# Kernel tuning notes

Hardware: AMD Instinct MI355X
Metric: run time of the kernel (lower is better)

The kernel has to match this reference:

```python
import jax, jax.numpy as jnp
import numpy as np

B, S1, S2, H, H2, D, K = 1, 1024, 8192, 32, 8, 128, 128


def setup_inputs() -> dict:
    key = jax.random.key(0)
    k1, k2, k3, k4 = jax.random.split(key, 4)
    q = jax.random.normal(k1, (B, S1, H, D), dtype=jnp.float16)
    k = jax.random.normal(k2, (B, S2, H2, D), dtype=jnp.float16)
    v = jax.random.normal(k3, (B, S2, H2, D), dtype=jnp.float16)
    sparse_indices = jax.random.randint(k4, (B, S1, H2, K), 0, S2, dtype=jnp.int32)
    return {"q": q, "k": k, "v": v, "sparse_indices": sparse_indices}


def reference(q, k, v, sparse_indices):
    # q: [B,S1,H,D]  k,v: [B,S2,H2,D]  sparse_indices: [B,S1,H2,K]
    b, s1, h, d = q.shape
    h2 = sparse_indices.shape[2]
    g = h // h2  # GQA group size
    scale = 1.0 / np.sqrt(d).astype(np.float32)
    qg = q.reshape(b, s1, h2, g, d)  # group queries per kv head
    b_idx = jnp.arange(b)[:, None, None, None]
    h_idx = jnp.arange(h2)[None, None, :, None]
    # gather per-query sparse KV sets: [B,S1,H2,K,D]
    kg = k[b_idx, sparse_indices, h_idx]
    vg = v[b_idx, sparse_indices, h_idx]
    scores = jnp.einsum('bshgd,bshkd->bshgk', qg, kg).astype(jnp.float32) * scale
    p = jax.nn.softmax(scores, axis=-1).astype(q.dtype)
    out = jnp.einsum('bshgk,bshkd->bshgd', p, vg)  # [B,S1,H2,G,D]
    return out.reshape(b, s1, h, d).astype(jnp.float16)
```

## Files before the change

### kernel.cpp

```cpp
#include <hip/hip_runtime.h>
#include <stdint.h>
#include <math.h>

#define NH 32
#define NH2 8
#define DD 128
#define KSEL 128
#define GG 4
#define S2MASK 8191

__global__ __launch_bounds__(256) void sparse_attn_kernel(
    const float* __restrict__ q, const float* __restrict__ k,
    const float* __restrict__ v, const int* __restrict__ idx,
    float* __restrict__ out) {
  __shared__ int sIdx[4][KSEL];
  __shared__ __align__(16) float sS[4][GG][KSEL];
  __shared__ __align__(16) float sP[4][KSEL][GG];

  const int tid = threadIdx.x;
  const int w = tid >> 6;
  const int lane = tid & 63;
  const int h2 = blockIdx.x & 7;
  const int s1 = ((blockIdx.x >> 3) << 2) + w;

  const int* ip = idx + (s1 * NH2 + h2) * KSEL;
  sIdx[w][lane]      = ip[lane] & S2MASK;
  sIdx[w][lane + 64] = ip[lane + 64] & S2MASK;

  const int c = lane & 15;
  const int r = lane >> 4;
  float4 qa[GG], qb[GG];
  const float* qp = q + (s1 * NH + h2 * GG) * DD + c * 8;
#pragma unroll
  for (int g = 0; g < GG; ++g) {
    qa[g] = *(const float4*)(qp + g * DD);
    qb[g] = *(const float4*)(qp + g * DD + 4);
  }

  __syncthreads();

  const float scale = 0.08838834764831845f;

#pragma unroll 4
  for (int it = 0; it < 32; ++it) {
    const int j = it * 4 + r;
    const int s2 = sIdx[w][j];
    const float* kp = k + (s2 * NH2 + h2) * DD + c * 8;
    const float4 ka = *(const float4*)(kp);
    const float4 kb = *(const float4*)(kp + 4);
    float sg0, sg1, sg2, sg3;
    {
      sg0 = qa[0].x * ka.x; sg1 = qa[1].x * ka.x;
      sg2 = qa[2].x * ka.x; sg3 = qa[3].x * ka.x;
      sg0 = fmaf(qa[0].y, ka.y, sg0); sg1 = fmaf(qa[1].y, ka.y, sg1);
      sg2 = fmaf(qa[2].y, ka.y, sg2); sg3 = fmaf(qa[3].y, ka.y, sg3);
      sg0 = fmaf(qa[0].z, ka.z, sg0); sg1 = fmaf(qa[1].z, ka.z, sg1);
      sg2 = fmaf(qa[2].z, ka.z, sg2); sg3 = fmaf(qa[3].z, ka.z, sg3);
      sg0 = fmaf(qa[0].w, ka.w, sg0); sg1 = fmaf(qa[1].w, ka.w, sg1);
      sg2 = fmaf(qa[2].w, ka.w, sg2); sg3 = fmaf(qa[3].w, ka.w, sg3);
      sg0 = fmaf(qb[0].x, kb.x, sg0); sg1 = fmaf(qb[1].x, kb.x, sg1);
      sg2 = fmaf(qb[2].x, kb.x, sg2); sg3 = fmaf(qb[3].x, kb.x, sg3);
      sg0 = fmaf(qb[0].y, kb.y, sg0); sg1 = fmaf(qb[1].y, kb.y, sg1);
      sg2 = fmaf(qb[2].y, kb.y, sg2); sg3 = fmaf(qb[3].y, kb.y, sg3);
      sg0 = fmaf(qb[0].z, kb.z, sg0); sg1 = fmaf(qb[1].z, kb.z, sg1);
      sg2 = fmaf(qb[2].z, kb.z, sg2); sg3 = fmaf(qb[3].z, kb.z, sg3);
      sg0 = fmaf(qb[0].w, kb.w, sg0); sg1 = fmaf(qb[1].w, kb.w, sg1);
      sg2 = fmaf(qb[2].w, kb.w, sg2); sg3 = fmaf(qb[3].w, kb.w, sg3);
    }
#pragma unroll
    for (int off = 1; off < 16; off <<= 1) {
      sg0 += __shfl_xor(sg0, off);
      sg1 += __shfl_xor(sg1, off);
      sg2 += __shfl_xor(sg2, off);
      sg3 += __shfl_xor(sg3, off);
    }
    float val = (c == 0) ? sg0 : (c == 1) ? sg1 : (c == 2) ? sg2 : sg3;
    if (c < GG) sS[w][c][j] = val * scale;
  }
  __syncthreads();

#pragma unroll
  for (int g = 0; g < GG; ++g) {
    float a0 = sS[w][g][lane];
    float a1 = sS[w][g][lane + 64];
    float m = fmaxf(a0, a1);
#pragma unroll
    for (int off = 32; off >= 1; off >>= 1) m = fmaxf(m, __shfl_xor(m, off));
    float e0 = expf(a0 - m);
    float e1 = expf(a1 - m);
    float s = e0 + e1;
#pragma unroll
    for (int off = 32; off >= 1; off >>= 1) s += __shfl_xor(s, off);
    const float inv = 1.0f / fmaxf(s, 1e-30f);
    sP[w][lane][g]      = e0 * inv;
    sP[w][lane + 64][g] = e1 * inv;
  }
  __syncthreads();

  float a00 = 0.f, a01 = 0.f, a10 = 0.f, a11 = 0.f;
  float a20 = 0.f, a21 = 0.f, a30 = 0.f, a31 = 0.f;
  const float* vb = v + h2 * DD + lane * 2;
#pragma unroll 8
  for (int j = 0; j < KSEL; ++j) {
    const int s2 = sIdx[w][j];
    const float2 vv = *(const float2*)(vb + (size_t)s2 * (NH2 * DD));
    const float4 p = *(const float4*)&sP[w][j][0];
    a00 = fmaf(p.x, vv.x, a00); a01 = fmaf(p.x, vv.y, a01);
    a10 = fmaf(p.y, vv.x, a10); a11 = fmaf(p.y, vv.y, a11);
    a20 = fmaf(p.z, vv.x, a20); a21 = fmaf(p.z, vv.y, a21);
    a30 = fmaf(p.w, vv.x, a30); a31 = fmaf(p.w, vv.y, a31);
  }

  float* op = out + (s1 * NH + h2 * GG) * DD + lane * 2;
  *(float2*)(op + 0 * DD) = make_float2(a00, a01);
  *(float2*)(op + 1 * DD) = make_float2(a10, a11);
  *(float2*)(op + 2 * DD) = make_float2(a20, a21);
  *(float2*)(op + 3 * DD) = make_float2(a30, a31);
}

extern "C" void kernel_launch(void* const* d_in, const int* in_sizes, int n_in,
                              void* d_out, int out_size, void* d_ws, size_t ws_size,
                              hipStream_t stream) {
  const float* q = (const float*)d_in[0];
  const float* k = (const float*)d_in[1];
  const float* v = (const float*)d_in[2];
  const int* idx = (const int*)d_in[3];
  float* out = (float*)d_out;
  sparse_attn_kernel<<<dim3(2048), dim3(256), 0, stream>>>(q, k, v, idx, out);
}
```

Before: 183.9 us.

## Compute QK scores with fp16 MFMA and vectorize softmax across group heads

Replaces the scalar FMA plus shuffle-reduction QK dot products with 16x16x32 fp16 MFMA instructions. Q (padded to 16 rows, only 4 used) and the gathered K rows are converted from fp32 to fp16 in registers. Scores are written straight into the sP buffer, which removes the separate sS array. The softmax now processes all four group heads at once with float4 and uses fast __expf. The change reduces ALU and shuffle work in the score phase, at the cost of wasted MFMA rows and fp16 rounding of K and Q.

```diff
diff --git a/kernel.cpp b/kernel.cpp
--- a/kernel.cpp
+++ b/kernel.cpp
@@ -9,12 +9,24 @@
 #define GG 4
 #define S2MASK 8191
 
+typedef _Float16 h8   __attribute__((ext_vector_type(8)));
+typedef __fp16   hp2  __attribute__((ext_vector_type(2)));
+typedef float    f32x4 __attribute__((ext_vector_type(4)));
+
+static __device__ __forceinline__ h8 cvt8(float4 a, float4 b) {
+  union { h8 v; hp2 p[4]; } u;
+  u.p[0] = __builtin_amdgcn_cvt_pkrtz(a.x, a.y);
+  u.p[1] = __builtin_amdgcn_cvt_pkrtz(a.z, a.w);
+  u.p[2] = __builtin_amdgcn_cvt_pkrtz(b.x, b.y);
+  u.p[3] = __builtin_amdgcn_cvt_pkrtz(b.z, b.w);
+  return u.v;
+}
+
 __global__ __launch_bounds__(256) void sparse_attn_kernel(
     const float* __restrict__ q, const float* __restrict__ k,
     const float* __restrict__ v, const int* __restrict__ idx,
     float* __restrict__ out) {
   __shared__ int sIdx[4][KSEL];
-  __shared__ __align__(16) float sS[4][GG][KSEL];
   __shared__ __align__(16) float sP[4][KSEL][GG];
 
   const int tid = threadIdx.x;
@@ -27,73 +39,77 @@
   sIdx[w][lane]      = ip[lane] & S2MASK;
   sIdx[w][lane + 64] = ip[lane + 64] & S2MASK;
 
-  const int c = lane & 15;
-  const int r = lane >> 4;
-  float4 qa[GG], qb[GG];
-  const float* qp = q + (s1 * NH + h2 * GG) * DD + c * 8;
+  const int m  = lane & 15;
+  const int kg = lane >> 4;
+
+  h8 aq[4];
 #pragma unroll
-  for (int g = 0; g < GG; ++g) {
-    qa[g] = *(const float4*)(qp + g * DD);
-    qb[g] = *(const float4*)(qp + g * DD + 4);
+  for (int t = 0; t < 4; ++t)
+#pragma unroll
+    for (int i = 0; i < 8; ++i) aq[t][i] = (_Float16)0;
+  if (m < GG) {
+    const float* qp = q + (s1 * NH + h2 * GG + m) * DD + kg * 8;
+#pragma unroll
+    for (int t = 0; t < 4; ++t) {
+      float4 f0 = *(const float4*)(qp + 32 * t);
+      float4 f1 = *(const float4*)(qp + 32 * t + 4);
+      aq[t] = cvt8(f0, f1);
+    }
   }
 
   __syncthreads();
 
   const float scale = 0.08838834764831845f;
 
-#pragma unroll 4
-  for (int it = 0; it < 32; ++it) {
-    const int j = it * 4 + r;
-    const int s2 = sIdx[w][j];
-    const float* kp = k + (s2 * NH2 + h2) * DD + c * 8;
-    const float4 ka = *(const float4*)(kp);
-    const float4 kb = *(const float4*)(kp + 4);
-    float sg0, sg1, sg2, sg3;
-    {
-      sg0 = qa[0].x * ka.x; sg1 = qa[1].x * ka.x;
-      sg2 = qa[2].x * ka.x; sg3 = qa[3].x * ka.x;
-      sg0 = fmaf(qa[0].y, ka.y, sg0); sg1 = fmaf(qa[1].y, ka.y, sg1);
-      sg2 = fmaf(qa[2].y, ka.y, sg2); sg3 = fmaf(qa[3].y, ka.y, sg3);
-      sg0 = fmaf(qa[0].z, ka.z, sg0); sg1 = fmaf(qa[1].z, ka.z, sg1);
-      sg2 = fmaf(qa[2].z, ka.z, sg2); sg3 = fmaf(qa[3].z, ka.z, sg3);
-      sg0 = fmaf(qa[0].w, ka.w, sg0); sg1 = fmaf(qa[1].w, ka.w, sg1);
-      sg2 = fmaf(qa[2].w, ka.w, sg2); sg3 = fmaf(qa[3].w, ka.w, sg3);
-      sg0 = fmaf(qb[0].x, kb.x, sg0); sg1 = fmaf(qb[1].x, kb.x, sg1);
-      sg2 = fmaf(qb[2].x, kb.x, sg2); sg3 = fmaf(qb[3].x, kb.x, sg3);
-      sg0 = fmaf(qb[0].y, kb.y, sg0); sg1 = fmaf(qb[1].y, kb.y, sg1);
-      sg2 = fmaf(qb[2].y, kb.y, sg2); sg3 = fmaf(qb[3].y, kb.y, sg3);
-      sg0 = fmaf(qb[0].z, kb.z, sg0); sg1 = fmaf(qb[1].z, kb.z, sg1);
-      sg2 = fmaf(qb[2].z, kb.z, sg2); sg3 = fmaf(qb[3].z, kb.z, sg3);
-      sg0 = fmaf(qb[0].w, kb.w, sg0); sg1 = fmaf(qb[1].w, kb.w, sg1);
-      sg2 = fmaf(qb[2].w, kb.w, sg2); sg3 = fmaf(qb[3].w, kb.w, sg3);
+#pragma unroll 2
+  for (int nt = 0; nt < 8; ++nt) {
+    const int s2 = sIdx[w][nt * 16 + m];
+    const float* kp = k + (s2 * NH2 + h2) * DD + kg * 8;
+    f32x4 acc = {0.f, 0.f, 0.f, 0.f};
+#pragma unroll
+    for (int t = 0; t < 4; ++t) {
+      float4 f0 = *(const float4*)(kp + 32 * t);
+      float4 f1 = *(const float4*)(kp + 32 * t + 4);
+      acc = __builtin_amdgcn_mfma_f32_16x16x32_f16(aq[t], cvt8(f0, f1), acc, 0, 0, 0);
     }
-#pragma unroll
-    for (int off = 1; off < 16; off <<= 1) {
-      sg0 += __shfl_xor(sg0, off);
-      sg1 += __shfl_xor(sg1, off);
-      sg2 += __shfl_xor(sg2, off);
-      sg3 += __shfl_xor(sg3, off);
+    if (lane < 16) {
+      float4 sc = make_float4(acc[0] * scale, acc[1] * scale,
+                              acc[2] * scale, acc[3] * scale);
+      *(float4*)&sP[w][nt * 16 + lane][0] = sc;
     }
-    float val = (c == 0) ? sg0 : (c == 1) ? sg1 : (c == 2) ? sg2 : sg3;
-    if (c < GG) sS[w][c][j] = val * scale;
   }
   __syncthreads();
 
+  {
+    float4 p0 = *(const float4*)&sP[w][lane][0];
+    float4 p1 = *(const float4*)&sP[w][lane + 64][0];
+    float4 mx = make_float4(fmaxf(p0.x, p1.x), fmaxf(p0.y, p1.y),
+                            fmaxf(p0.z, p1.z), fmaxf(p0.w, p1.w));
 #pragma unroll
-  for (int g = 0; g < GG; ++g) {
-    float a0 = sS[w][g][lane];
-    float a1 = sS[w][g][lane + 64];
-    float m = fmaxf(a0, a1);
+    for (int off = 1; off < 64; off <<= 1) {
+      mx.x = fmaxf(mx.x, __shfl_xor(mx.x, off));
+      mx.y = fmaxf(mx.y, __shfl_xor(mx.y, off));
+      mx.z = fmaxf(mx.z, __shfl_xor(mx.z, off));
+      mx.w = fmaxf(mx.w, __shfl_xor(mx.w, off));
+    }
+    float4 e0 = make_float4(__expf(p0.x - mx.x), __expf(p0.y - mx.y),
+                            __expf(p0.z - mx.z), __expf(p0.w - mx.w));
+    float4 e1 = make_float4(__expf(p1.x - mx.x), __expf(p1.y - mx.y),
+                            __expf(p1.z - mx.z), __expf(p1.w - mx.w));
+    float4 sm = make_float4(e0.x + e1.x, e0.y + e1.y, e0.z + e1.z, e0.w + e1.w);
 #pragma unroll
-    for (int off = 32; off >= 1; off >>= 1) m = fmaxf(m, __shfl_xor(m, off));
-    float e0 = expf(a0 - m);
-    float e1 = expf(a1 - m);
-    float s = e0 + e1;
-#pragma unroll
-    for (int off = 32; off >= 1; off >>= 1) s += __shfl_xor(s, off);
-    const float inv = 1.0f / fmaxf(s, 1e-30f);
-    sP[w][lane][g]      = e0 * inv;
-    sP[w][lane + 64][g] = e1 * inv;
+    for (int off = 1; off < 64; off <<= 1) {
+      sm.x += __shfl_xor(sm.x, off);
+      sm.y += __shfl_xor(sm.y, off);
+      sm.z += __shfl_xor(sm.z, off);
+      sm.w += __shfl_xor(sm.w, off);
+    }
+    float4 inv = make_float4(1.f / fmaxf(sm.x, 1e-30f), 1.f / fmaxf(sm.y, 1e-30f),
+                             1.f / fmaxf(sm.z, 1e-30f), 1.f / fmaxf(sm.w, 1e-30f));
+    *(float4*)&sP[w][lane][0] =
+        make_float4(e0.x * inv.x, e0.y * inv.y, e0.z * inv.z, e0.w * inv.w);
+    *(float4*)&sP[w][lane + 64][0] =
+        make_float4(e1.x * inv.x, e1.y * inv.y, e1.z * inv.z, e1.w * inv.w);
   }
   __syncthreads();
 
```

Result: slower. 194.2 us (+5.6%).
